# Kernel tuning notes

Hardware: AMD Instinct MI355X
Metric: run time of the kernel (lower is better)

Reference implementation:

```python
import jax, jax.numpy as jnp
import numpy as np

INIT_DIM = 512
HID = 1024
OUT = 64
N_NODES = 100000
N_NBR = 65536


def setup_inputs() -> dict:
    key = jax.random.key(0)
    ks = jax.random.split(key, 12)
    inp = {}
    inp["feat"] = jax.random.normal(ks[0], (1, INIT_DIM), dtype=jnp.float32)
    for i, t in enumerate("abc"):
        inp[f"all_feat_{t}"] = jax.random.normal(ks[1 + i], (N_NODES, INIT_DIM), dtype=jnp.float32)
        inp[f"nbr_{t}"] = jax.random.randint(ks[4 + i], (N_NBR,), 0, N_NODES)
        inp[f"W1_{t}"] = jax.random.normal(ks[7 + i], (HID, INIT_DIM), dtype=jnp.float32) * 0.02
        inp[f"b1_{t}"] = jnp.zeros((HID,), dtype=jnp.float32)
    inp["Wc"] = jax.random.normal(ks[10], (OUT, HID), dtype=jnp.float32) * 0.02
    inp["bc"] = jnp.zeros((OUT,), dtype=jnp.float32)
    return inp


def reference(feat, all_feat_a, all_feat_b, all_feat_c,
              nbr_a, nbr_b, nbr_c,
              W1_a, b1_a, W1_b, b1_b, W1_c, b1_c, Wc, bc):
    # trans1 = 'rel-linear': per-type neighbor gather + relation-specific Linear
    # h_j: [N_NBR, HID]
    h_a = all_feat_a[nbr_a] @ W1_a.T + b1_a
    h_b = all_feat_b[nbr_b] @ W1_b.T + b1_b
    h_c = all_feat_c[nbr_c] @ W1_c.T + b1_c
    # trans2 = 'none' (passthrough); concat aggregation over all types
    h = jnp.concatenate([h_a, h_b, h_c], axis=0)  # [3*N_NBR, HID]
    h = jax.nn.relu(h)                             # activate = 'relu'
    pooled = h.mean(axis=0)                        # agg_node = 'mean' -> [HID]
    feat_all = jax.nn.relu(pooled)
    logits = feat_all @ Wc.T + bc                  # [OUT]
    return logits
```

## Files before the change

kernel.cpp:

```cpp
#include <hip/hip_runtime.h>
#include <hip/hip_bf16.h>

typedef __attribute__((ext_vector_type(4))) float f32x4;
typedef __attribute__((ext_vector_type(4))) int   int4v;
typedef __attribute__((ext_vector_type(2))) int   int2v;
typedef __attribute__((ext_vector_type(16))) int  i32x16;

#define N_NBR 65536
#define INIT_DIM 512
#define HID 1024
#define NTILE 3072
#define SA 24.0f
#define SW 1024.0f
#define INVS (1.0f / (24.0f * 1024.0f))

static __device__ __forceinline__ int q8(float x, float s) {
  float y = fminf(fmaxf(x * s, -127.f), 127.f);
  return __float2int_rn(y);
}
static __device__ __forceinline__ int pack4(float a, float b, float c, float d, float s) {
  return (q8(a,s) & 255) | ((q8(b,s) & 255) << 8) | ((q8(c,s) & 255) << 16) | ((q8(d,s) & 255) << 24);
}

__global__ __launch_bounds__(256) void k_convw(const float* __restrict__ wa,
                                               const float* __restrict__ wb,
                                               const float* __restrict__ wc,
                                               char* __restrict__ out) {
  int g = blockIdx.x * 256 + threadIdx.x;
  int l = g & 63;
  int blk = g >> 6;
  int ks = blk & 15;
  int nb = (blk >> 4) & 31;
  int t = blk >> 9;
  const float* src = (t == 0) ? wa : (t == 1) ? wb : wc;
  int n = nb * 32 + (l & 31);
  int k0 = ks * 32 + (l >> 5) * 16;
  const f32x4* p = (const f32x4*)(src + (size_t)n * INIT_DIM + k0);
  f32x4 x0 = p[0], x1 = p[1], x2 = p[2], x3 = p[3];
  int4v v;
  v[0] = pack4(x0.x, x0.y, x0.z, x0.w, SW);
  v[1] = pack4(x1.x, x1.y, x1.z, x1.w, SW);
  v[2] = pack4(x2.x, x2.y, x2.z, x2.w, SW);
  v[3] = pack4(x3.x, x3.y, x3.z, x3.w, SW);
  *(int4v*)(out + (size_t)g * 16) = v;
}

__global__ __launch_bounds__(256) void k_main(
    const float* __restrict__ fa, const float* __restrict__ fb, const float* __restrict__ fc,
    const int* __restrict__ na, const int* __restrict__ nb_, const int* __restrict__ nc__,
    const float* __restrict__ b1a, const float* __restrict__ b1b, const float* __restrict__ b1c,
    const char* __restrict__ wbf8,
    float* __restrict__ partials) {
  __shared__ __align__(16) char Asm[64 * 512];

  int bx = blockIdx.x;
  int t = bx >> 10;
  int mtile = bx & 1023;
  const float* feat = (t == 0) ? fa : (t == 1) ? fb : fc;
  const int*   nbr  = (t == 0) ? na : (t == 1) ? nb_ : nc__;
  const float* bias = (t == 0) ? b1a : (t == 1) ? b1b : b1c;
  const char*  Wf8  = wbf8 + (size_t)t * (32 * 16 * 1024);

  int tid = threadIdx.x;
  int wave = tid >> 6;
  int lane = tid & 63;
  int l31 = lane & 31, hi = lane >> 5;

  #pragma unroll 2
  for (int c = 0; c < 16; ++c) {
    int r = c * 4 + wave;
    int idx = nbr[mtile * 64 + r];
    const float* rp = feat + (size_t)idx * INIT_DIM + lane * 8;
    f32x4 a  = *(const f32x4*)rp;
    f32x4 b2 = *((const f32x4*)rp + 1);
    int2v v;
    v[0] = pack4(a.x, a.y, a.z, a.w, SA);
    v[1] = pack4(b2.x, b2.y, b2.z, b2.w, SA);
    unsigned byte = (unsigned)r * 512u +
                    (((unsigned)lane * 8u) ^ ((unsigned)(r & 31) << 4));
    *(int2v*)(Asm + byte) = v;
  }
  __syncthreads();

  unsigned swz = (unsigned)l31 << 4;
  unsigned abase = (unsigned)l31 * 512u + (((unsigned)hi << 4) ^ (swz & 16u));
  unsigned swzhi = swz & 0x1E0u;

  #pragma unroll
  for (int p = 0; p < 8; ++p) {
    const char* pB = Wf8 + ((size_t)(wave * 8 + p) << 14) + lane * 16;

    i32x16 acc[2] = {};
    #pragma unroll 4
    for (int ks = 0; ks < 16; ++ks) {
      int4v Bf = *(const int4v*)(pB + (ks << 10));
      unsigned kcol = (((unsigned)ks << 5) ^ swzhi);
      #pragma unroll
      for (int i = 0; i < 2; ++i) {
        int4v Af = *(const int4v*)(Asm + (abase + (unsigned)(i * 16384) + kcol));
        acc[i] = __builtin_amdgcn_mfma_i32_32x32x32_i8(Af, Bf, acc[i], 0, 0, 0);
      }
    }

    int n = (wave * 8 + p) * 32 + l31;
    int bq = __float2int_rn(bias[n] * (SA * SW));
    int s = 0;
    #pragma unroll
    for (int i = 0; i < 2; ++i)
      #pragma unroll
      for (int r = 0; r < 16; ++r)
        s += max(acc[i][r] + bq, 0);
    s += __shfl_xor(s, 32);
    if (hi == 0) partials[(size_t)bx * HID + n] = (float)s * INVS;
  }
}

__global__ __launch_bounds__(256) void k_reduce1(const float* __restrict__ partials,
                                                 float* __restrict__ inter) {
  int b = blockIdx.x;
  int tid = threadIdx.x;
  const f32x4* base = (const f32x4*)(partials + (size_t)b * 16 * HID) + tid;
  f32x4 s = {0.f, 0.f, 0.f, 0.f};
  #pragma unroll 4
  for (int r = 0; r < 16; ++r) {
    f32x4 v = base[r * (HID / 4)];
    s.x += v.x; s.y += v.y; s.z += v.z; s.w += v.w;
  }
  *((f32x4*)(inter + (size_t)b * HID) + tid) = s;
}

__global__ __launch_bounds__(1024) void k_reduce2(const float* __restrict__ inter,
                                                  float* __restrict__ acc) {
  int col = threadIdx.x;
  float s = 0.f;
  #pragma unroll 8
  for (int r = 0; r < 192; ++r) s += inter[(size_t)r * HID + col];
  acc[col] = s;
}

__global__ __launch_bounds__(256) void k_final(const float* __restrict__ acc,
                                               const float* __restrict__ Wc,
                                               const float* __restrict__ bc,
                                               float* __restrict__ out) {
  __shared__ float fall[HID];
  int tid = threadIdx.x;
  const float inv = 1.f / (3.f * (float)N_NBR);
  for (int i = tid; i < HID; i += 256) {
    float p = acc[i] * inv;
    fall[i] = (p > 0.f) ? p : 0.f;
  }
  __syncthreads();
  int o = tid >> 2, q = tid & 3;
  const f32x4* w = (const f32x4*)(Wc + (size_t)o * HID + q * 256);
  const f32x4* f = (const f32x4*)(fall + q * 256);
  float s = 0.f;
  #pragma unroll 4
  for (int k = 0; k < 64; ++k) {
    f32x4 wv = w[k], fv = f[k];
    s += wv.x * fv.x + wv.y * fv.y + wv.z * fv.z + wv.w * fv.w;
  }
  s += __shfl_xor(s, 1);
  s += __shfl_xor(s, 2);
  if (q == 0) out[o] = s + bc[o];
}

extern "C" void kernel_launch(void* const* d_in, const int* in_sizes, int n_in,
                              void* d_out, int out_size, void* d_ws, size_t ws_size,
                              hipStream_t stream) {
  const float* fa  = (const float*)d_in[1];
  const int*   na  = (const int*)d_in[2];
  const float* W1a = (const float*)d_in[3];
  const float* b1a = (const float*)d_in[4];
  const float* fb  = (const float*)d_in[5];
  const int*   nb  = (const int*)d_in[6];
  const float* W1b = (const float*)d_in[7];
  const float* b1b = (const float*)d_in[8];
  const float* fc  = (const float*)d_in[9];
  const int*   nc  = (const int*)d_in[10];
  const float* W1c = (const float*)d_in[11];
  const float* b1c = (const float*)d_in[12];
  const float* Wc  = (const float*)d_in[13];
  const float* bc  = (const float*)d_in[14];
  float* out = (float*)d_out;

  float* acc = (float*)d_ws;
  char*  wbf8 = (char*)d_ws + 4096;
  float* partials = (float*)((char*)d_ws + 4096 + 3 * 32 * 16 * 1024);
  float* inter = partials + (size_t)NTILE * HID;

  k_convw<<<384, 256, 0, stream>>>(W1a, W1b, W1c, wbf8);
  k_main<<<NTILE, 256, 0, stream>>>(fa, fb, fc, na, nb, nc, b1a, b1b, b1c, wbf8, partials);
  k_reduce1<<<192, 256, 0, stream>>>(partials, inter);
  k_reduce2<<<1, 1024, 0, stream>>>(inter, acc);
  k_final<<<1, 256, 0, stream>>>(acc, Wc, bc, out);
}
```

Before: 181.1 us.

## Re-tile main GEMM waves as 2x2 grid sharing A fragments across two B columns

Waves are rearranged from each covering all 64 rows for a quarter of the columns into a 2x2 layout: each wave covers 32 rows and half the columns. Each LDS A fragment is reused across two MFMAs with different B tiles, replacing two A reads per B fragment. The cost is twice the global B loads per wave, plus a shared-memory buffer and an extra barrier to combine row-half partial sums before the store.

```diff
diff --git a/kernel.cpp b/kernel.cpp
--- a/kernel.cpp
+++ b/kernel.cpp
@@ -52,6 +52,7 @@
     const char* __restrict__ wbf8,
     float* __restrict__ partials) {
   __shared__ __align__(16) char Asm[64 * 512];
+  __shared__ float csum[2][2][512];
 
   int bx = blockIdx.x;
   int t = bx >> 10;
@@ -63,6 +64,8 @@
 
   int tid = threadIdx.x;
   int wave = tid >> 6;
+  int wr = wave >> 1;
+  int wc = wave & 1;
   int lane = tid & 63;
   int l31 = lane & 31, hi = lane >> 5;
 
@@ -83,35 +86,44 @@
   __syncthreads();
 
   unsigned swz = (unsigned)l31 << 4;
-  unsigned abase = (unsigned)l31 * 512u + (((unsigned)hi << 4) ^ (swz & 16u));
+  unsigned abase = (unsigned)(wr * 32 + l31) * 512u +
+                   (((unsigned)hi << 4) ^ (swz & 16u));
   unsigned swzhi = swz & 0x1E0u;
 
   #pragma unroll
   for (int p = 0; p < 8; ++p) {
-    const char* pB = Wf8 + ((size_t)(wave * 8 + p) << 14) + lane * 16;
+    const char* pBa = Wf8 + ((size_t)(wc * 16 + p * 2)     << 14) + lane * 16;
+    const char* pBb = Wf8 + ((size_t)(wc * 16 + p * 2 + 1) << 14) + lane * 16;
 
     i32x16 acc[2] = {};
     #pragma unroll 4
     for (int ks = 0; ks < 16; ++ks) {
-      int4v Bf = *(const int4v*)(pB + (ks << 10));
-      unsigned kcol = (((unsigned)ks << 5) ^ swzhi);
-      #pragma unroll
-      for (int i = 0; i < 2; ++i) {
-        int4v Af = *(const int4v*)(Asm + (abase + (unsigned)(i * 16384) + kcol));
-        acc[i] = __builtin_amdgcn_mfma_i32_32x32x32_i8(Af, Bf, acc[i], 0, 0, 0);
-      }
+      int4v Bf0 = *(const int4v*)(pBa + (ks << 10));
+      int4v Bf1 = *(const int4v*)(pBb + (ks << 10));
+      int4v Af = *(const int4v*)(Asm + (abase + (((unsigned)ks << 5) ^ swzhi)));
+      acc[0] = __builtin_amdgcn_mfma_i32_32x32x32_i8(Af, Bf0, acc[0], 0, 0, 0);
+      acc[1] = __builtin_amdgcn_mfma_i32_32x32x32_i8(Af, Bf1, acc[1], 0, 0, 0);
     }
 
-    int n = (wave * 8 + p) * 32 + l31;
-    int bq = __float2int_rn(bias[n] * (SA * SW));
-    int s = 0;
     #pragma unroll
-    for (int i = 0; i < 2; ++i)
+    for (int j = 0; j < 2; ++j) {
+      int n = (wc * 16 + p * 2 + j) * 32 + l31;
+      int bq = __float2int_rn(bias[n] * (SA * SW));
+      int s = 0;
       #pragma unroll
       for (int r = 0; r < 16; ++r)
-        s += max(acc[i][r] + bq, 0);
-    s += __shfl_xor(s, 32);
-    if (hi == 0) partials[(size_t)bx * HID + n] = (float)s * INVS;
+        s += max(acc[j][r] + bq, 0);
+      s += __shfl_xor(s, 32);
+      if (hi == 0) csum[wr][wc][(p * 2 + j) * 32 + l31] = (float)s * INVS;
+    }
+  }
+  __syncthreads();
+
+  #pragma unroll
+  for (int g = 0; g < 4; ++g) {
+    int col = g * 256 + tid;
+    int w2 = col >> 9, loc = col & 511;
+    partials[(size_t)bx * HID + col] = csum[0][w2][loc] + csum[1][w2][loc];
   }
 }
 
```

Result: slower. 203.3 us (+12.3%).
